# Optimization experiments

Measured on AMD Instinct MI355X. Metric: run time of the kernel, lower is better.

The kernel has to match this reference:

```python
import jax, jax.numpy as jnp
import numpy as np

N, E, DIN, DOUT = 10000, 640000, 128, 256
BN_EPS = 1e-5
GIN_EPS = 0.0  # GINConv default eps, train_eps=False


def setup_inputs() -> dict:
    key = jax.random.key(0)
    ks = jax.random.split(key, 10)
    x = jax.random.normal(ks[0], (N, DIN), dtype=jnp.float32)
    edge_index = jax.random.randint(ks[1], (2, E), 0, N, dtype=jnp.int64)
    s1 = 1.0 / np.sqrt(DIN)
    s2 = 1.0 / np.sqrt(DOUT)
    return {
        "x": x,
        "edge_index": edge_index,
        "W1": jax.random.uniform(ks[2], (DIN, DOUT), jnp.float32, -s1, s1),
        "b1": jax.random.uniform(ks[3], (DOUT,), jnp.float32, -s1, s1),
        "gamma1": jnp.ones((DOUT,), jnp.float32),
        "beta1": jnp.zeros((DOUT,), jnp.float32),
        "W2": jax.random.uniform(ks[4], (DOUT, DOUT), jnp.float32, -s2, s2),
        "b2": jax.random.uniform(ks[5], (DOUT,), jnp.float32, -s2, s2),
        "gamma2": jnp.ones((DOUT,), jnp.float32),
        "beta2": jnp.zeros((DOUT,), jnp.float32),
    }


def _batchnorm(h, gamma, beta):
    # training-mode BatchNorm1d: batch statistics, biased variance
    mean = jnp.mean(h, axis=0)
    var = jnp.mean(jnp.square(h - mean), axis=0)
    return gamma * (h - mean) * jax.lax.rsqrt(var + BN_EPS) + beta


def reference(x, edge_index, W1, b1, gamma1, beta1, W2, b2, gamma2, beta2):
    src, dst = edge_index[0], edge_index[1]
    # GINConv: out_i = MLP((1+eps)*x_i + sum_{j->i} x_j)
    agg = jax.ops.segment_sum(x[src], dst, num_segments=N)  # [N, DIN]
    h = (1.0 + GIN_EPS) * x + agg
    # MLP: Linear -> BN -> ReLU -> Linear
    h = h @ W1 + b1
    h = jax.nn.relu(_batchnorm(h, gamma1, beta1))
    h = h @ W2 + b2
    # outer BN + ReLU
    return jax.nn.relu(_batchnorm(h, gamma2, beta2))
```

## Files before the change

kernel.cpp:

```cpp
#include <hip/hip_runtime.h>

#define NN 10000
#define DIN 128
#define DOUT 256
#define NB 128
#define PAD 192
#define NTILES (NN / 16)
static constexpr float BN_EPS = 1e-5f;

using short8 = __attribute__((ext_vector_type(8))) short;
using f32x4  = __attribute__((ext_vector_type(4))) float;

__device__ __forceinline__ unsigned short bf16r(float f) {
    unsigned int u = __float_as_uint(f);
    u += 0x7FFFu + ((u >> 16) & 1u);
    return (unsigned short)(u >> 16);
}
__device__ __forceinline__ float bf16f(unsigned short h) {
    return __uint_as_float((unsigned int)h << 16);
}
__device__ __forceinline__ int fragidx(int k, int n) {
    return ((k >> 5) << 13) | ((n >> 4) << 9) |
           ((((k >> 3) & 3) << 4 | (n & 15)) << 3) | (k & 7);
}

__global__ __launch_bounds__(256) void khist_prep(
    const int* __restrict__ ei, ushort* __restrict__ hist_g,
    ushort* __restrict__ rank, int E,
    const float* __restrict__ x, ushort* __restrict__ xb,
    const float* __restrict__ W1, ushort* __restrict__ w1f,
    const float* __restrict__ W2, ushort* __restrict__ w2f,
    float* __restrict__ stats) {
    const int tid = threadIdx.x;
    if (blockIdx.x < NB) {
        __shared__ int hist[NN];
        for (int i = tid; i < NN; i += 256) hist[i] = 0;
        __syncthreads();
        const int chunk = (E + NB - 1) / NB;
        const int e0 = blockIdx.x * chunk;
        const int e1 = min(e0 + chunk, E);
        for (int e = e0 + tid; e < e1; e += 256) {
            rank[e] = (ushort)atomicAdd(&hist[ei[E + e]], 1);
        }
        __syncthreads();
        ushort* dst = hist_g + (size_t)blockIdx.x * NN;
        for (int i = tid; i < NN; i += 256) dst[i] = (ushort)hist[i];
    } else {
        const int pt = (blockIdx.x - NB) * 256 + tid;
        if (pt < 8192) stats[pt] = 0.f;
        for (int i = pt; i < NN * DIN / 4; i += 32768) {
            const float4 v = reinterpret_cast<const float4*>(x)[i];
            ushort4 o;
            o.x = bf16r(v.x); o.y = bf16r(v.y);
            o.z = bf16r(v.z); o.w = bf16r(v.w);
            reinterpret_cast<ushort4*>(xb)[i] = o;
        }
        {
            const int k = pt >> 8, n = pt & 255;
            w1f[fragidx(k, n)] = bf16r(W1[pt]);
        }
        for (int i = pt; i < 256 * 256; i += 32768) {
            const int k = i >> 8, n = i & 255;
            w2f[fragidx(k, n)] = bf16r(W2[i]);
        }
    }
}

__global__ __launch_bounds__(256) void kscan_a(ushort* __restrict__ hist_g,
                                               int* __restrict__ total) {
    const int node = blockIdx.x * 256 + threadIdx.x;
    if (node >= NN) return;
    int run = 0;
#pragma unroll 8
    for (int b = 0; b < NB; ++b) {
        const int v = hist_g[(size_t)b * NN + node];
        hist_g[(size_t)b * NN + node] = (ushort)run;
        run += v;
    }
    total[node] = run;
}

__global__ __launch_bounds__(256) void kfill(const int* __restrict__ ei,
                                             const ushort* __restrict__ hist_g,
                                             const ushort* __restrict__ rank,
                                             int* __restrict__ edge_src,
                                             int E) {
    const int chunk = (E + NB - 1) / NB;
    for (int e = blockIdx.x * 256 + threadIdx.x; e < E;
         e += gridDim.x * 256) {
        const int src = ei[e];
        const int dst = ei[E + e];
        const int b = e / chunk;
        const int pos = dst * PAD + (int)hist_g[(size_t)b * NN + dst]
                        + (int)rank[e];
        edge_src[pos] = src;
    }
}

__global__ __launch_bounds__(256) void gemm1_k(
    const float* __restrict__ x, const ushort* __restrict__ xb,
    const int* __restrict__ total, const int* __restrict__ edge_src,
    const ushort* __restrict__ w1f, const float* __restrict__ b1,
    ushort* __restrict__ h1f, float* __restrict__ sum1,
    float* __restrict__ sq1) {
    __shared__ short a_lds[4 * 64 * 8];
    __shared__ float work[6208];
    short* b_lds = (short*)work;
    float* hrow  = work;
    float* red_s = work + 4160;
    float* red_q = work + 5184;
    const int tid = threadIdx.x;
    const int w = tid >> 6, l = tid & 63;
    const int m = blockIdx.x;
    const int hw = tid >> 5, c4 = tid & 31;
    const ushort4* xb4 = reinterpret_cast<const ushort4*>(xb);

#pragma unroll
    for (int r = 0; r < 2; ++r) {
        const int row = r * 8 + hw;
        const int node = m * 16 + row;
        const int beg = node * PAD;
        const int end = beg + total[node];

        float4 a0 = make_float4(0.f, 0.f, 0.f, 0.f);
        float4 a1 = a0, a2 = a0, a3 = a0;
        int j = beg;
        for (; j + 7 < end; j += 8) {
            int s[8];
#pragma unroll
            for (int t = 0; t < 8; ++t) s[t] = edge_src[j + t];
            ushort4 v[8];
#pragma unroll
            for (int t = 0; t < 8; ++t) v[t] = xb4[(size_t)s[t] * 32 + c4];
#pragma unroll
            for (int t = 0; t < 8; ++t) {
                float4* a = (t & 3) == 0 ? &a0 : (t & 3) == 1 ? &a1
                          : (t & 3) == 2 ? &a2 : &a3;
                a->x += bf16f(v[t].x);
                a->y += bf16f(v[t].y);
                a->z += bf16f(v[t].z);
                a->w += bf16f(v[t].w);
            }
        }
        for (; j < end; ++j) {
            const ushort4 v = xb4[(size_t)edge_src[j] * 32 + c4];
            a0.x += bf16f(v.x); a0.y += bf16f(v.y);
            a0.z += bf16f(v.z); a0.w += bf16f(v.w);
        }
        const float4 xv =
            reinterpret_cast<const float4*>(x)[(size_t)node * 32 + c4];
        ushort4 o;
        o.x = bf16r(xv.x + a0.x + a1.x + a2.x + a3.x);
        o.y = bf16r(xv.y + a0.y + a1.y + a2.y + a3.y);
        o.z = bf16r(xv.z + a0.z + a1.z + a2.z + a3.z);
        o.w = bf16r(xv.w + a0.w + a1.w + a2.w + a3.w);
        const int c = c4 >> 3, kg = (c4 >> 1) & 3, half = c4 & 1;
        *reinterpret_cast<ushort4*>(
            (char*)a_lds + c * 1024 + ((kg << 4) + row) * 16 + half * 8) = o;
    }

    f32x4 acc[4];
#pragma unroll
    for (int p = 0; p < 4; ++p) {
        const float b = b1[(w * 4 + p) * 16 + (l & 15)];
        acc[p] = (f32x4){b, b, b, b};
    }

    for (int c = 0; c < 4; ++c) {
        __syncthreads();
        const float4* src = ((const float4*)w1f) + c * 1024;
#pragma unroll
        for (int i = 0; i < 4; ++i)
            ((float4*)b_lds)[tid + 256 * i] = src[tid + 256 * i];
        __syncthreads();
        const short8 a = ((const short8*)a_lds)[c * 64 + l];
#pragma unroll
        for (int p = 0; p < 4; ++p) {
            const short8 b = ((const short8*)b_lds)[(w * 4 + p) * 64 + l];
            acc[p] = __builtin_amdgcn_mfma_f32_16x16x32_bf16(a, b, acc[p],
                                                             0, 0, 0);
        }
    }
    __syncthreads();

#pragma unroll
    for (int p = 0; p < 4; ++p) {
        const int col = (w * 4 + p) * 16 + (l & 15);
        float s = 0.f, q = 0.f;
#pragma unroll
        for (int r = 0; r < 4; ++r) {
            const float v = acc[p][r];
            hrow[((l >> 4) * 4 + r) * 260 + col] = v;
            s += v;
            q += v * v;
        }
        red_s[(l >> 4) * 256 + col] = s;
        red_q[(l >> 4) * 256 + col] = q;
    }
    __syncthreads();
    {
        float s = 0.f, q = 0.f;
#pragma unroll
        for (int g = 0; g < 4; ++g) {
            s += red_s[g * 256 + tid];
            q += red_q[g * 256 + tid];
        }
        atomicAdd(&sum1[(m & 7) * 256 + tid], s);
        atomicAdd(&sq1[(m & 7) * 256 + tid], q);
    }
#pragma unroll
    for (int t = 0; t < 2; ++t) {
        const int u = tid + t * 256;
        const int c2 = u >> 6, kg = (u >> 4) & 3, row = u & 15;
        const float* src = &hrow[row * 260 + c2 * 32 + kg * 8];
        short8 g;
#pragma unroll
        for (int jj = 0; jj < 8; ++jj) g[jj] = (short)bf16r(src[jj]);
        ((short8*)h1f)[m * 512 + u] = g;
    }
}

__global__ __launch_bounds__(256) void gemm2_k(
    const ushort* __restrict__ h1f, const float* __restrict__ sum1,
    const float* __restrict__ sq1, const float* __restrict__ gamma1,
    const float* __restrict__ beta1, const ushort* __restrict__ w2f,
    const float* __restrict__ b2, float* __restrict__ h2,
    float* __restrict__ sum2, float* __restrict__ sq2) {
    __shared__ short a_lds[8 * 64 * 8];
    __shared__ float work[6208];
    __shared__ float sc1[DOUT], sh1[DOUT];
    short* b_lds = (short*)work;
    float* hrow  = work;
    float* red_s = work + 4160;
    float* red_q = work + 5184;
    const int tid = threadIdx.x;
    const int w = tid >> 6, l = tid & 63;
    const int m = blockIdx.x;

    {
        float s = 0.f, q = 0.f;
#pragma unroll
        for (int i = 0; i < 8; ++i) {
            s += sum1[i * 256 + tid];
            q += sq1[i * 256 + tid];
        }
        const float nInv = 1.0f / (float)NN;
        const float mean = s * nInv;
        const float var = q * nInv - mean * mean;
        const float sc = gamma1[tid] * rsqrtf(var + BN_EPS);
        sc1[tid] = sc;
        sh1[tid] = beta1[tid] - mean * sc;
    }
    __syncthreads();

#pragma unroll
    for (int t = 0; t < 2; ++t) {
        const int u = tid + 256 * t;
        const int col0 = ((u >> 6) << 5) + (((u >> 4) & 3) << 3);
        const short8 hv = ((const short8*)h1f)[m * 512 + u];
        short8 g;
#pragma unroll
        for (int jj = 0; jj < 8; ++jj) {
            const float f = bf16f((unsigned short)hv[jj]);
            const float r = fmaxf(fmaf(f, sc1[col0 + jj], sh1[col0 + jj]), 0.f);
            g[jj] = (short)bf16r(r);
        }
        ((short8*)a_lds)[u] = g;
    }

    f32x4 acc[4];
#pragma unroll
    for (int p = 0; p < 4; ++p) {
        const float b = b2[(w * 4 + p) * 16 + (l & 15)];
        acc[p] = (f32x4){b, b, b, b};
    }

    for (int c = 0; c < 8; ++c) {
        __syncthreads();
        const float4* src = ((const float4*)w2f) + c * 1024;
#pragma unroll
        for (int i = 0; i < 4; ++i)
            ((float4*)b_lds)[tid + 256 * i] = src[tid + 256 * i];
        __syncthreads();
        const short8 a = ((const short8*)a_lds)[c * 64 + l];
#pragma unroll
        for (int p = 0; p < 4; ++p) {
            const short8 b = ((const short8*)b_lds)[(w * 4 + p) * 64 + l];
            acc[p] = __builtin_amdgcn_mfma_f32_16x16x32_bf16(a, b, acc[p],
                                                             0, 0, 0);
        }
    }
    __syncthreads();

#pragma unroll
    for (int p = 0; p < 4; ++p) {
        const int col = (w * 4 + p) * 16 + (l & 15);
        float s = 0.f, q = 0.f;
#pragma unroll
        for (int r = 0; r < 4; ++r) {
            const float v = acc[p][r];
            hrow[((l >> 4) * 4 + r) * 260 + col] = v;
            s += v;
            q += v * v;
        }
        red_s[(l >> 4) * 256 + col] = s;
        red_q[(l >> 4) * 256 + col] = q;
    }
    __syncthreads();
    {
        float s = 0.f, q = 0.f;
#pragma unroll
        for (int g = 0; g < 4; ++g) {
            s += red_s[g * 256 + tid];
            q += red_q[g * 256 + tid];
        }
        atomicAdd(&sum2[(m & 7) * 256 + tid], s);
        atomicAdd(&sq2[(m & 7) * 256 + tid], q);
    }
#pragma unroll
    for (int i = 0; i < 4; ++i) {
        const int idx = tid + 256 * i;
        const int row = idx >> 6, col4 = idx & 63;
        const float4 v = *(const float4*)&hrow[row * 260 + col4 * 4];
        ((float4*)h2)[(size_t)(m * 16 + row) * 64 + col4] = v;
    }
}

__global__ __launch_bounds__(256) void bn_relu_out_k(
    const float* __restrict__ h2, const float* __restrict__ sum2,
    const float* __restrict__ sq2, const float* __restrict__ gamma2,
    const float* __restrict__ beta2, float* __restrict__ out) {
    __shared__ float sc2[DOUT], sh2[DOUT];
    const int tid = threadIdx.x;
    {
        float s = 0.f, q = 0.f;
#pragma unroll
        for (int i = 0; i < 8; ++i) {
            s += sum2[i * 256 + tid];
            q += sq2[i * 256 + tid];
        }
        const float nInv = 1.0f / (float)NN;
        const float mean = s * nInv;
        const float var = q * nInv - mean * mean;
        const float sc = gamma2[tid] * rsqrtf(var + BN_EPS);
        sc2[tid] = sc;
        sh2[tid] = beta2[tid] - mean * sc;
    }
    __syncthreads();
#pragma unroll
    for (int i = 0; i < 4; ++i) {
        const int u = blockIdx.x * 1024 + i * 256 + tid;
        const int k4 = u & 63;
        const float4 h = reinterpret_cast<const float4*>(h2)[u];
        const float4 sc = reinterpret_cast<const float4*>(sc2)[k4];
        const float4 sh = reinterpret_cast<const float4*>(sh2)[k4];
        float4 g;
        g.x = fmaxf(fmaf(h.x, sc.x, sh.x), 0.f);
        g.y = fmaxf(fmaf(h.y, sc.y, sh.y), 0.f);
        g.z = fmaxf(fmaf(h.z, sc.z, sh.z), 0.f);
        g.w = fmaxf(fmaf(h.w, sc.w, sh.w), 0.f);
        reinterpret_cast<float4*>(out)[u] = g;
    }
}

extern "C" void kernel_launch(void* const* d_in, const int* in_sizes, int n_in,
                              void* d_out, int out_size, void* d_ws,
                              size_t ws_size, hipStream_t stream) {
    const float* x      = (const float*)d_in[0];
    const int*   ei     = (const int*)d_in[1];
    const float* W1     = (const float*)d_in[2];
    const float* b1     = (const float*)d_in[3];
    const float* gamma1 = (const float*)d_in[4];
    const float* beta1  = (const float*)d_in[5];
    const float* W2     = (const float*)d_in[6];
    const float* b2     = (const float*)d_in[7];
    const float* gamma2 = (const float*)d_in[8];
    const float* beta2  = (const float*)d_in[9];
    const int E = in_sizes[1] / 2;

    char* w = (char*)d_ws;
    size_t off = 0;
    float* stats = (float*)(w + off); off += 32768;
    float* sum1 = stats + 0;
    float* sq1  = stats + 2048;
    float* sum2 = stats + 4096;
    float* sq2  = stats + 6144;
    ushort* hist_g = (ushort*)(w + off); off += (size_t)NB * NN * 2;
    ushort* rank   = (ushort*)(w + off); off += (size_t)E * 2;
    int* total    = (int*)(w + off); off += 40064;
    int* edge_src = (int*)(w + off); off += (size_t)NN * PAD * 4;
    ushort* xb    = (ushort*)(w + off); off += (size_t)NN * DIN * 2;
    ushort* w1f   = (ushort*)(w + off); off += 65536;
    ushort* w2f   = (ushort*)(w + off); off += 131072;
    ushort* h1f   = (ushort*)(w + off); off += (size_t)NN * DOUT * 2;
    float* h2     = (float*)(w + off); off += (size_t)NN * DOUT * 4;
    float* out    = (float*)d_out;

    khist_prep<<<2 * NB, 256, 0, stream>>>(ei, hist_g, rank, E, x, xb,
                                           W1, w1f, W2, w2f, stats);
    kscan_a<<<40, 256, 0, stream>>>(hist_g, total);
    kfill<<<256, 256, 0, stream>>>(ei, hist_g, rank, edge_src, E);
    gemm1_k<<<NTILES, 256, 0, stream>>>(x, xb, total, edge_src, w1f, b1,
                                        h1f, sum1, sq1);
    gemm2_k<<<NTILES, 256, 0, stream>>>(h1f, sum1, sq1, gamma1, beta1, w2f,
                                        b2, h2, sum2, sq2);
    bn_relu_out_k<<<NN * DOUT / 4 / 1024, 256, 0, stream>>>(h2, sum2, sq2,
                                                            gamma2, beta2, out);
}
```

Measured before the change: 79.35 us.

## Use 512-thread GEMM blocks, store h2 as bf16, halve histogram blocks

Gemm1 and gemm2 now run 512 threads per 16-row tile. In gemm1 each half-warp gathers one node's neighbours, and each wave computes two 16-column MFMA tiles instead of four. The intermediate h2 is stored as bf16 instead of fp32, which halves its write and read traffic in the final BN kernel but adds rounding error. The histogram phase uses 64 edge blocks instead of 128, which shortens the scan but lengthens each block's edge chunk.

Result: faster. 74.29 us (-6.4%).

```diff
diff --git a/kernel.cpp b/kernel.cpp
--- a/kernel.cpp
+++ b/kernel.cpp
@@ -3,7 +3,8 @@
 #define NN 10000
 #define DIN 128
 #define DOUT 256
-#define NB 128
+#define NB 64
+#define NPREP 128
 #define PAD 192
 #define NTILES (NN / 16)
 static constexpr float BN_EPS = 1e-5f;
@@ -48,7 +49,7 @@
     } else {
         const int pt = (blockIdx.x - NB) * 256 + tid;
         if (pt < 8192) stats[pt] = 0.f;
-        for (int i = pt; i < NN * DIN / 4; i += 32768) {
+        for (int i = pt; i < NN * DIN / 4; i += NPREP * 256) {
             const float4 v = reinterpret_cast<const float4*>(x)[i];
             ushort4 o;
             o.x = bf16r(v.x); o.y = bf16r(v.y);
@@ -59,7 +60,7 @@
             const int k = pt >> 8, n = pt & 255;
             w1f[fragidx(k, n)] = bf16r(W1[pt]);
         }
-        for (int i = pt; i < 256 * 256; i += 32768) {
+        for (int i = pt; i < 256 * 256; i += NPREP * 256) {
             const int k = i >> 8, n = i & 255;
             w2f[fragidx(k, n)] = bf16r(W2[i]);
         }
@@ -97,7 +98,7 @@
     }
 }
 
-__global__ __launch_bounds__(256) void gemm1_k(
+__global__ __launch_bounds__(512) void gemm1_k(
     const float* __restrict__ x, const ushort* __restrict__ xb,
     const int* __restrict__ total, const int* __restrict__ edge_src,
     const ushort* __restrict__ w1f, const float* __restrict__ b1,
@@ -115,38 +116,33 @@
     const int hw = tid >> 5, c4 = tid & 31;
     const ushort4* xb4 = reinterpret_cast<const ushort4*>(xb);
 
-#pragma unroll
-    for (int r = 0; r < 2; ++r) {
-        const int row = r * 8 + hw;
-        const int node = m * 16 + row;
-        const int beg = node * PAD;
-        const int end = beg + total[node];
-
-        float4 a0 = make_float4(0.f, 0.f, 0.f, 0.f);
-        float4 a1 = a0, a2 = a0, a3 = a0;
-        int j = beg;
-        for (; j + 7 < end; j += 8) {
-            int s[8];
-#pragma unroll
-            for (int t = 0; t < 8; ++t) s[t] = edge_src[j + t];
-            ushort4 v[8];
-#pragma unroll
-            for (int t = 0; t < 8; ++t) v[t] = xb4[(size_t)s[t] * 32 + c4];
-#pragma unroll
-            for (int t = 0; t < 8; ++t) {
-                float4* a = (t & 3) == 0 ? &a0 : (t & 3) == 1 ? &a1
-                          : (t & 3) == 2 ? &a2 : &a3;
-                a->x += bf16f(v[t].x);
-                a->y += bf16f(v[t].y);
-                a->z += bf16f(v[t].z);
-                a->w += bf16f(v[t].w);
-            }
-        }
-        for (; j < end; ++j) {
-            const ushort4 v = xb4[(size_t)edge_src[j] * 32 + c4];
-            a0.x += bf16f(v.x); a0.y += bf16f(v.y);
-            a0.z += bf16f(v.z); a0.w += bf16f(v.w);
-        }
+    const int node = m * 16 + hw;
+    const int beg = node * PAD, end = beg + total[node];
+    float4 a0 = make_float4(0.f, 0.f, 0.f, 0.f);
+    float4 a1 = a0, a2 = a0, a3 = a0;
+    int j = beg;
+    for (; j + 3 < end; j += 4) {
+        int s[4];
+#pragma unroll
+        for (int t = 0; t < 4; ++t) s[t] = edge_src[j + t];
+        ushort4 v[4];
+#pragma unroll
+        for (int t = 0; t < 4; ++t) v[t] = xb4[(size_t)s[t] * 32 + c4];
+        a0.x += bf16f(v[0].x); a0.y += bf16f(v[0].y);
+        a0.z += bf16f(v[0].z); a0.w += bf16f(v[0].w);
+        a1.x += bf16f(v[1].x); a1.y += bf16f(v[1].y);
+        a1.z += bf16f(v[1].z); a1.w += bf16f(v[1].w);
+        a2.x += bf16f(v[2].x); a2.y += bf16f(v[2].y);
+        a2.z += bf16f(v[2].z); a2.w += bf16f(v[2].w);
+        a3.x += bf16f(v[3].x); a3.y += bf16f(v[3].y);
+        a3.z += bf16f(v[3].z); a3.w += bf16f(v[3].w);
+    }
+    for (; j < end; ++j) {
+        const ushort4 v = xb4[(size_t)edge_src[j] * 32 + c4];
+        a0.x += bf16f(v.x); a0.y += bf16f(v.y);
+        a0.z += bf16f(v.z); a0.w += bf16f(v.w);
+    }
+    {
         const float4 xv =
             reinterpret_cast<const float4*>(x)[(size_t)node * 32 + c4];
         ushort4 o;
@@ -156,27 +152,27 @@
         o.w = bf16r(xv.w + a0.w + a1.w + a2.w + a3.w);
         const int c = c4 >> 3, kg = (c4 >> 1) & 3, half = c4 & 1;
         *reinterpret_cast<ushort4*>(
-            (char*)a_lds + c * 1024 + ((kg << 4) + row) * 16 + half * 8) = o;
-    }
-
-    f32x4 acc[4];
-#pragma unroll
-    for (int p = 0; p < 4; ++p) {
-        const float b = b1[(w * 4 + p) * 16 + (l & 15)];
+            (char*)a_lds + c * 1024 + ((kg << 4) + hw) * 16 + half * 8) = o;
+    }
+
+    f32x4 acc[2];
+#pragma unroll
+    for (int p = 0; p < 2; ++p) {
+        const float b = b1[(w * 2 + p) * 16 + (l & 15)];
         acc[p] = (f32x4){b, b, b, b};
     }
 
-    for (int c = 0; c < 4; ++c) {
-        __syncthreads();
-        const float4* src = ((const float4*)w1f) + c * 1024;
-#pragma unroll
-        for (int i = 0; i < 4; ++i)
-            ((float4*)b_lds)[tid + 256 * i] = src[tid + 256 * i];
-        __syncthreads();
-        const short8 a = ((const short8*)a_lds)[c * 64 + l];
-#pragma unroll
-        for (int p = 0; p < 4; ++p) {
-            const short8 b = ((const short8*)b_lds)[(w * 4 + p) * 64 + l];
+    for (int cc = 0; cc < 4; ++cc) {
+        __syncthreads();
+        const float4* src = ((const float4*)w1f) + cc * 1024;
+#pragma unroll
+        for (int i = 0; i < 2; ++i)
+            ((float4*)b_lds)[tid + 512 * i] = src[tid + 512 * i];
+        __syncthreads();
+        const short8 a = ((const short8*)a_lds)[cc * 64 + l];
+#pragma unroll
+        for (int p = 0; p < 2; ++p) {
+            const short8 b = ((const short8*)b_lds)[(w * 2 + p) * 64 + l];
             acc[p] = __builtin_amdgcn_mfma_f32_16x16x32_bf16(a, b, acc[p],
                                                              0, 0, 0);
         }
@@ -184,8 +180,8 @@
     __syncthreads();
 
 #pragma unroll
-    for (int p = 0; p < 4; ++p) {
-        const int col = (w * 4 + p) * 16 + (l & 15);
+    for (int p = 0; p < 2; ++p) {
+        const int col = (w * 2 + p) * 16 + (l & 15);
         float s = 0.f, q = 0.f;
 #pragma unroll
         for (int r = 0; r < 4; ++r) {
@@ -198,21 +194,22 @@
         red_q[(l >> 4) * 256 + col] = q;
     }
     __syncthreads();
+    if (tid < 256) {
+        float s = 0.f;
+#pragma unroll
+        for (int g = 0; g < 4; ++g) s += red_s[g * 256 + tid];
+        atomicAdd(&sum1[(m & 7) * 256 + tid], s);
+    } else {
+        const int col = tid - 256;
+        float q = 0.f;
+#pragma unroll
+        for (int g = 0; g < 4; ++g) q += red_q[g * 256 + col];
+        atomicAdd(&sq1[(m & 7) * 256 + col], q);
+    }
     {
-        float s = 0.f, q = 0.f;
-#pragma unroll
-        for (int g = 0; g < 4; ++g) {
-            s += red_s[g * 256 + tid];
-            q += red_q[g * 256 + tid];
-        }
-        atomicAdd(&sum1[(m & 7) * 256 + tid], s);
-        atomicAdd(&sq1[(m & 7) * 256 + tid], q);
-    }
-#pragma unroll
-    for (int t = 0; t < 2; ++t) {
-        const int u = tid + t * 256;
-        const int c2 = u >> 6, kg = (u >> 4) & 3, row = u & 15;
-        const float* src = &hrow[row * 260 + c2 * 32 + kg * 8];
+        const int u = tid;
+        const int c2 = u >> 6, kg2 = (u >> 4) & 3, row = u & 15;
+        const float* src = &hrow[row * 260 + c2 * 32 + kg2 * 8];
         short8 g;
 #pragma unroll
         for (int jj = 0; jj < 8; ++jj) g[jj] = (short)bf16r(src[jj]);
@@ -220,11 +217,11 @@
     }
 }
 
-__global__ __launch_bounds__(256) void gemm2_k(
+__global__ __launch_bounds__(512) void gemm2_k(
     const ushort* __restrict__ h1f, const float* __restrict__ sum1,
     const float* __restrict__ sq1, const float* __restrict__ gamma1,
     const float* __restrict__ beta1, const ushort* __restrict__ w2f,
-    const float* __restrict__ b2, float* __restrict__ h2,
+    const float* __restrict__ b2, ushort* __restrict__ h2b,
     float* __restrict__ sum2, float* __restrict__ sq2) {
     __shared__ short a_lds[8 * 64 * 8];
     __shared__ float work[6208];
@@ -237,7 +234,7 @@
     const int w = tid >> 6, l = tid & 63;
     const int m = blockIdx.x;
 
-    {
+    if (tid < 256) {
         float s = 0.f, q = 0.f;
 #pragma unroll
         for (int i = 0; i < 8; ++i) {
@@ -253,9 +250,8 @@
     }
     __syncthreads();
 
-#pragma unroll
-    for (int t = 0; t < 2; ++t) {
-        const int u = tid + 256 * t;
+    {
+        const int u = tid;
         const int col0 = ((u >> 6) << 5) + (((u >> 4) & 3) << 3);
         const short8 hv = ((const short8*)h1f)[m * 512 + u];
         short8 g;
@@ -268,10 +264,10 @@
         ((short8*)a_lds)[u] = g;
     }
 
-    f32x4 acc[4];
-#pragma unroll
-    for (int p = 0; p < 4; ++p) {
-        const float b = b2[(w * 4 + p) * 16 + (l & 15)];
+    f32x4 acc[2];
+#pragma unroll
+    for (int p = 0; p < 2; ++p) {
+        const float b = b2[(w * 2 + p) * 16 + (l & 15)];
         acc[p] = (f32x4){b, b, b, b};
     }
 
@@ -279,13 +275,13 @@
         __syncthreads();
         const float4* src = ((const float4*)w2f) + c * 1024;
 #pragma unroll
-        for (int i = 0; i < 4; ++i)
-            ((float4*)b_lds)[tid + 256 * i] = src[tid + 256 * i];
+        for (int i = 0; i < 2; ++i)
+            ((float4*)b_lds)[tid + 512 * i] = src[tid + 512 * i];
         __syncthreads();
         const short8 a = ((const short8*)a_lds)[c * 64 + l];
 #pragma unroll
-        for (int p = 0; p < 4; ++p) {
-            const short8 b = ((const short8*)b_lds)[(w * 4 + p) * 64 + l];
+        for (int p = 0; p < 2; ++p) {
+            const short8 b = ((const short8*)b_lds)[(w * 2 + p) * 64 + l];
             acc[p] = __builtin_amdgcn_mfma_f32_16x16x32_bf16(a, b, acc[p],
                                                              0, 0, 0);
         }
@@ -293,8 +289,8 @@
     __syncthreads();
 
 #pragma unroll
-    for (int p = 0; p < 4; ++p) {
-        const int col = (w * 4 + p) * 16 + (l & 15);
+    for (int p = 0; p < 2; ++p) {
+        const int col = (w * 2 + p) * 16 + (l & 15);
         float s = 0.f, q = 0.f;
 #pragma unroll
         for (int r = 0; r < 4; ++r) {
@@ -307,27 +303,36 @@
         red_q[(l >> 4) * 256 + col] = q;
     }
     __syncthreads();
+    if (tid < 256) {
+        float s = 0.f;
+#pragma unroll
+        for (int g = 0; g < 4; ++g) s += red_s[g * 256 + tid];
+        atomicAdd(&sum2[(m & 7) * 256 + tid], s);
+    } else {
+        const int col = tid - 256;
+        float q = 0.f;
+#pragma unroll
+        for (int g = 0; g < 4; ++g) q += red_q[g * 256 + col];
+        atomicAdd(&sq2[(m & 7) * 256 + col], q);
+    }
     {
-        float s = 0.f, q = 0.f;
-#pragma unroll
-        for (int g = 0; g < 4; ++g) {
-            s += red_s[g * 256 + tid];
-            q += red_q[g * 256 + tid];
-        }
-        atomicAdd(&sum2[(m & 7) * 256 + tid], s);
-        atomicAdd(&sq2[(m & 7) * 256 + tid], q);
-    }
-#pragma unroll
-    for (int i = 0; i < 4; ++i) {
-        const int idx = tid + 256 * i;
-        const int row = idx >> 6, col4 = idx & 63;
-        const float4 v = *(const float4*)&hrow[row * 260 + col4 * 4];
-        ((float4*)h2)[(size_t)(m * 16 + row) * 64 + col4] = v;
+        const int idx = tid;
+        const int row = idx >> 5, col8 = idx & 31;
+        const float* src = &hrow[row * 260 + col8 * 8];
+        ushort4 lo, hi;
+        lo.x = bf16r(src[0]); lo.y = bf16r(src[1]);
+        lo.z = bf16r(src[2]); lo.w = bf16r(src[3]);
+        hi.x = bf16r(src[4]); hi.y = bf16r(src[5]);
+        hi.z = bf16r(src[6]); hi.w = bf16r(src[7]);
+        reinterpret_cast<ushort4*>(h2b)[((size_t)(m * 16 + row) * 64 +
+                                         col8 * 2)] = lo;
+        reinterpret_cast<ushort4*>(h2b)[((size_t)(m * 16 + row) * 64 +
+                                         col8 * 2 + 1)] = hi;
     }
 }
 
 __global__ __launch_bounds__(256) void bn_relu_out_k(
-    const float* __restrict__ h2, const float* __restrict__ sum2,
+    const ushort* __restrict__ h2b, const float* __restrict__ sum2,
     const float* __restrict__ sq2, const float* __restrict__ gamma2,
     const float* __restrict__ beta2, float* __restrict__ out) {
     __shared__ float sc2[DOUT], sh2[DOUT];
@@ -351,14 +356,14 @@
     for (int i = 0; i < 4; ++i) {
         const int u = blockIdx.x * 1024 + i * 256 + tid;
         const int k4 = u & 63;
-        const float4 h = reinterpret_cast<const float4*>(h2)[u];
+        const ushort4 hv = reinterpret_cast<const ushort4*>(h2b)[u];
         const float4 sc = reinterpret_cast<const float4*>(sc2)[k4];
         const float4 sh = reinterpret_cast<const float4*>(sh2)[k4];
         float4 g;
-        g.x = fmaxf(fmaf(h.x, sc.x, sh.x), 0.f);
-        g.y = fmaxf(fmaf(h.y, sc.y, sh.y), 0.f);
-        g.z = fmaxf(fmaf(h.z, sc.z, sh.z), 0.f);
-        g.w = fmaxf(fmaf(h.w, sc.w, sh.w), 0.f);
+        g.x = fmaxf(fmaf(bf16f(hv.x), sc.x, sh.x), 0.f);
+        g.y = fmaxf(fmaf(bf16f(hv.y), sc.y, sh.y), 0.f);
+        g.z = fmaxf(fmaf(bf16f(hv.z), sc.z, sh.z), 0.f);
+        g.w = fmaxf(fmaf(bf16f(hv.w), sc.w, sh.w), 0.f);
         reinterpret_cast<float4*>(out)[u] = g;
     }
 }
@@ -393,17 +398,17 @@
     ushort* w1f   = (ushort*)(w + off); off += 65536;
     ushort* w2f   = (ushort*)(w + off); off += 131072;
     ushort* h1f   = (ushort*)(w + off); off += (size_t)NN * DOUT * 2;
-    float* h2     = (float*)(w + off); off += (size_t)NN * DOUT * 4;
+    ushort* h2b   = (ushort*)(w + off); off += (size_t)NN * DOUT * 2;
     float* out    = (float*)d_out;
 
-    khist_prep<<<2 * NB, 256, 0, stream>>>(ei, hist_g, rank, E, x, xb,
-                                           W1, w1f, W2, w2f, stats);
+    khist_prep<<<NB + NPREP, 256, 0, stream>>>(ei, hist_g, rank, E, x, xb,
+                                               W1, w1f, W2, w2f, stats);
     kscan_a<<<40, 256, 0, stream>>>(hist_g, total);
     kfill<<<256, 256, 0, stream>>>(ei, hist_g, rank, edge_src, E);
-    gemm1_k<<<NTILES, 256, 0, stream>>>(x, xb, total, edge_src, w1f, b1,
+    gemm1_k<<<NTILES, 512, 0, stream>>>(x, xb, total, edge_src, w1f, b1,
                                         h1f, sum1, sq1);
-    gemm2_k<<<NTILES, 256, 0, stream>>>(h1f, sum1, sq1, gamma1, beta1, w2f,
-                                        b2, h2, sum2, sq2);
-    bn_relu_out_k<<<NN * DOUT / 4 / 1024, 256, 0, stream>>>(h2, sum2, sq2,
+    gemm2_k<<<NTILES, 512, 0, stream>>>(h1f, sum1, sq1, gamma1, beta1, w2f,
+                                        b2, h2b, sum2, sq2);
+    bn_relu_out_k<<<NN * DOUT / 4 / 1024, 256, 0, stream>>>(h2b, sum2, sq2,
                                                             gamma2, beta2, out);
 }
```
